# Kernel tuning notes

Hardware: AMD Instinct MI355X
Metric: run time of the kernel (lower is better)

The kernel has to match this reference:

```python
import jax, jax.numpy as jnp
import numpy as np

B, S, E, H = 8, 1024, 1024, 16
D = E // H            # head_dim = 64
L = 1024              # pos_max_len; rpe table rows = 2*L+1
SCALE = D ** 0.5


def setup_inputs() -> dict:
    key = jax.random.key(0)
    ks = jax.random.split(key, 7)
    x = jax.random.normal(ks[0], (B, S, E), dtype=jnp.float32)
    mask = jnp.tril(jnp.ones((S, S), dtype=bool))[None, None]  # causal [1,1,S,S]
    w = 1.0 / np.sqrt(E)
    Wq = jax.random.normal(ks[1], (E, E), dtype=jnp.float32) * w
    Wk = jax.random.normal(ks[2], (E, E), dtype=jnp.float32) * w
    Wv = jax.random.normal(ks[3], (E, E), dtype=jnp.float32) * w
    Wo = jax.random.normal(ks[4], (E, E), dtype=jnp.float32) * w
    pek_table = jax.random.normal(ks[5], (2 * L + 1, D), dtype=jnp.float32) / D ** 0.5
    pev_table = jax.random.normal(ks[6], (2 * L + 1, D), dtype=jnp.float32) / D ** 0.5
    return {"x": x, "mask": mask, "Wq": Wq, "Wk": Wk, "Wv": Wv, "Wo": Wo,
            "pek_table": pek_table, "pev_table": pev_table}


def reference(x, mask, Wq, Wk, Wv, Wo, pek_table, pev_table):
    # QKV projections (torch Linear: y = x @ W.T), reshaped to [B,H,S,D]
    q = (x @ Wq.T).reshape(B, S, H, D).transpose(0, 2, 1, 3)
    k = (x @ Wk.T).reshape(B, S, H, D).transpose(0, 2, 1, 3)
    v = (x @ Wv.T).reshape(B, S, H, D).transpose(0, 2, 1, 3)

    scores = jnp.einsum('bhsd,bhtd->bhst', q, k) / SCALE  # [B,H,S,S]

    # relative-position embeddings: rel[i,j] selects embedding for offset j-i
    pos = jnp.arange(S)
    rel = jnp.clip(pos[None, :] - pos[:, None] + L, 0, 2 * L)  # [S,S]
    pek = pek_table[rel]  # [S,S,D]
    pev = pev_table[rel]  # [S,S,D]

    # RPE score term, replicating torch view/transpose semantics exactly:
    # Q2: [B,S,H,D] -> [S,B,H,D] -> [S, B*H, D]
    q2 = (x @ Wq.T).reshape(B, S, H, D).transpose(1, 0, 2, 3).reshape(S, B * H, D)
    s2 = jnp.einsum('snd,std->snt', q2, pek)               # [S, B*H, S]
    s2 = s2.reshape(S, H, B, S).transpose(2, 1, 0, 3)      # torch .view(S,H,B,S).transpose(0,2)
    scores = scores + s2 / SCALE

    scores = jnp.where(mask, scores, -jnp.inf)
    attn = jax.nn.softmax(scores, axis=-1)                  # [B,H,S,S]

    out = jnp.einsum('bhst,bhtd->bhsd', attn, v)            # [B,H,S,D]

    # RPE value term: attn.transpose(0,2) -> [S,H,B,S] -> [S, H*B, S]
    a2 = attn.transpose(2, 1, 0, 3).reshape(S, H * B, S)
    o2 = jnp.einsum('snt,std->snd', a2, pev)                # [S, H*B, D]
    o2 = o2.reshape(S, H, B, D).transpose(2, 1, 0, 3)       # [B,H,S,D]
    out = out + o2

    out = out.transpose(0, 2, 1, 3).reshape(B, S, E) @ Wo.T
    return out
```

## Files before the change

kernel.cpp:

```cpp
#include <hip/hip_runtime.h>
#include <math.h>

#define NB 8
#define NS 1024
#define NE 1024
#define NH 16
#define ND 64
#define NL 1024

typedef __attribute__((ext_vector_type(8))) short short8;
typedef __attribute__((ext_vector_type(4))) float f32x4;
typedef __attribute__((ext_vector_type(16))) float f32x16;

__device__ __forceinline__ ushort f2bf(float f) {
    union { __bf16 h; ushort u; } v;
    v.h = (__bf16)f;
    return v.u;
}
__device__ __forceinline__ float bf2f(ushort u) {
    union { unsigned u; float f; } v; v.u = ((unsigned)u) << 16;
    return v.f;
}

__device__ __forceinline__ void stage16(const ushort* gsrc, ushort* lbase) {
    __builtin_amdgcn_global_load_lds((const __attribute__((address_space(1))) void*)gsrc,
                                     (__attribute__((address_space(3))) void*)lbase,
                                     16, 0, 0);
}

__global__ __launch_bounds__(256)
void cast_f2b4(const float* __restrict__ in, ushort* __restrict__ out, int n4) {
    int i = blockIdx.x * 256 + threadIdx.x;
    if (i >= n4) return;
    float4 v = ((const float4*)in)[i];
    ((ushort4*)out)[i] = make_ushort4(f2bf(v.x), f2bf(v.y), f2bf(v.z), f2bf(v.w));
}

__global__ __launch_bounds__(256)
void cast_w4(const float* __restrict__ Wq, const float* __restrict__ Wk,
             const float* __restrict__ Wv, const float* __restrict__ Wo,
             ushort* __restrict__ out) {
    int i = blockIdx.x * 256 + threadIdx.x;
    const int seg = i >> 18, j = i & 262143;
    const float* src = seg == 0 ? Wq : seg == 1 ? Wk : seg == 2 ? Wv : Wo;
    float4 v = ((const float4*)src)[j];
    ((ushort4*)out)[i] = make_ushort4(f2bf(v.x), f2bf(v.y), f2bf(v.z), f2bf(v.w));
}

__global__ __launch_bounds__(256)
void cast_pek(const float* __restrict__ pek, ushort* __restrict__ out, int n) {
    int i = blockIdx.x * 256 + threadIdx.x;
    if (i >= n) return;
    const int r = i >> 6, d = i & 63;
    out[(size_t)(d >> 4) * 32784 + (size_t)r * 16 + (d & 15)] = f2bf(pek[i]);
}

__global__ __launch_bounds__(256)
void cast_pevt(const float* __restrict__ pev, ushort* __restrict__ out) {
    int i = blockIdx.x * 256 + threadIdx.x;
    if (i >= 64 * 1056) return;
    const int d = i / 1056, r = i % 1056;
    const int m = r >> 5, cc = (r >> 4) & 1, hi = (r >> 3) & 1, j = r & 7;
    const int a = d >> 5, sl = d & 31;
    out[(size_t)m * 2048 + cc * 1024 + a * 512 + (sl * 2 + hi) * 8 + j] =
        f2bf(pev[(size_t)(r + 1) * ND + d]);
}

template<int MODE>
__global__ __launch_bounds__(256)
void gemm_mfma(const ushort* __restrict__ A, const ushort* __restrict__ W,
               float* __restrict__ Cf, ushort* __restrict__ Cb)
{
    constexpr int K = 1024;
    __shared__ __align__(16) ushort As[128 * 32];
    __shared__ __align__(16) ushort Bs[128 * 32];
    const int tid = threadIdx.x;
    const int w   = tid >> 6;
    const int l   = tid & 63;
    const int m0  = blockIdx.x * 128;
    const int n0  = blockIdx.y * 128;
    const int wr  = w >> 1, wc = w & 1;

    const int srow = 16 * w + (l >> 2);
    const int scol = (l & 3) * 8;
    const ushort* aptr = A + (size_t)(m0 + srow) * K + scol;
    const ushort* bptr = W + (size_t)(n0 + srow) * K + scol;
    ushort* asl = &As[w * 512];
    ushort* bsl = &Bs[w * 512];

    const int fl = l & 15, fk = (l >> 4) * 8;

    f32x4 acc[4][4] = {};

    for (int k0 = 0; k0 < K; k0 += 32) {
        __syncthreads();
        stage16(aptr + k0,                    asl);
        stage16(aptr + k0 + (size_t)64 * K,   asl + 2048);
        stage16(bptr + k0,                    bsl);
        stage16(bptr + k0 + (size_t)64 * K,   bsl + 2048);
        __syncthreads();

        short8 af[4], bf[4];
        #pragma unroll
        for (int i = 0; i < 4; ++i)
            af[i] = *(const short8*)&As[(wr * 64 + i * 16 + fl) * 32 + fk];
        #pragma unroll
        for (int j = 0; j < 4; ++j)
            bf[j] = *(const short8*)&Bs[(wc * 64 + j * 16 + fl) * 32 + fk];
        #pragma unroll
        for (int i = 0; i < 4; ++i)
            #pragma unroll
            for (int j = 0; j < 4; ++j)
                acc[i][j] = __builtin_amdgcn_mfma_f32_16x16x32_bf16(af[i], bf[j], acc[i][j], 0, 0, 0);
    }

    #pragma unroll
    for (int i = 0; i < 4; ++i) {
        #pragma unroll
        for (int j = 0; j < 4; ++j) {
            #pragma unroll
            for (int q = 0; q < 4; ++q) {
                const int m = m0 + wr * 64 + i * 16 + (l >> 4) * 4 + q;
                const int n = n0 + wc * 64 + j * 16 + fl;
                const float vv = acc[i][j][q];
                if (MODE == 0) {
                    const int b = m >> 10, s = m & 1023, h = n >> 6, d = n & 63;
                    Cb[(((size_t)b * NH + h) * NS + s) * ND + d] = f2bf(vv);
                } else if (MODE == 4) {
                    const int bh = (m >> 10) * 16 + (n >> 6), t = m & 1023, d = n & 63;
                    Cb[((size_t)bh * 4 + (d >> 4)) * 16384 + (size_t)t * 16 + (d & 15)] = f2bf(vv);
                } else if (MODE == 3) {
                    const int h = m >> 6, d = m & 63, b = n >> 10, s = n & 1023;
                    const int bh = b * 16 + h;
                    const int it = s >> 5, trel = s & 31;
                    const int c = trel >> 4, hi = (trel >> 3) & 1, jj = trel & 7;
                    const int a = d >> 5, sl = d & 31;
                    Cb[(size_t)bh * 65536 + it * 2048 +
                       ((a * 2 + c) * 64 + sl * 2 + hi) * 8 + jj] = f2bf(vv);
                } else {
                    Cf[(size_t)m * NE + n] = vv;
                }
            }
        }
    }
}

__global__ __launch_bounds__(64, 2)
void attn_mfma(const ushort* __restrict__ Qb, const ushort* __restrict__ Kf_,
               const ushort* __restrict__ Vf_, const ushort* __restrict__ PEKf,
               const ushort* __restrict__ PEVf, ushort* __restrict__ AO)
{
    const int idx = blockIdx.x;
    const int st  = 31 - (idx >> 7);
    const int bh  = idx & 127;
    const int b   = bh >> 4, h = bh & 15;
    const int n2  = h * NB + b;
    const int b2  = n2 >> 4, h2 = n2 & 15;
    const int s0  = st * 32;

    const int lane = threadIdx.x;
    const int sl   = lane & 31;
    const int hi   = lane >> 5;

    __shared__ __align__(16) ushort Mb[2][32][67];
    __shared__ __align__(16) ushort Pb[2][32][72];

    for (int t = lane; t < 2 * 32 * 72 / 2; t += 64) ((int*)Pb)[t] = 0;

    const ushort* qptr  = Qb + (((size_t)bh * NS) + s0 + sl) * ND + hi * 8;
    const ushort* q2ptr = Qb + ((((size_t)b2 * NH + h2) * NS) + s0 + sl) * ND + hi * 8;
    short8 qf[4], q2f[4];
    #pragma unroll
    for (int c = 0; c < 4; ++c) {
        qf[c]  = *(const short8*)(qptr  + 16 * c);
        q2f[c] = *(const short8*)(q2ptr + 16 * c);
    }

    const ushort* kfb  = Kf_ + (size_t)bh * 65536 + sl * 16 + hi * 8;
    const ushort* vfb  = Vf_ + (size_t)bh * 65536 + (sl * 2 + hi) * 8;
    const ushort* efb  = PEKf + sl * 16 + hi * 8;
    const ushort* pevw = PEVf + (size_t)(31 - st) * 2048 + (sl * 2 + hi) * 8;
    const int RBASE = NL - 31 - s0;

    auto mchunk = [&](int c, int dual, const short8* ef) {
        f32x16 cm = {};
        #pragma unroll
        for (int c4 = 0; c4 < 4; ++c4)
            cm = __builtin_amdgcn_mfma_f32_32x32x16_bf16(q2f[c4], ef[c4], cm, 0, 0, 0);
        #pragma unroll
        for (int q = 0; q < 16; ++q) {
            const int srow = (q & 3) + 8 * (q >> 2) + 4 * hi;
            const ushort bb = f2bf(cm[q]);
            Mb[c & 1][srow][sl] = bb;
            if (dual) Mb[(c + 1) & 1][srow][32 + sl] = bb;
        }
    };

    f32x16 acc0 = {}, acc1 = {};
    float mrow = -1e30f, lrow = 0.f;
    short8 kf[4], va[2][2], ea[4][2], efn[4];

    {
        short8 e0[4], e1[4];
        #pragma unroll
        for (int c4 = 0; c4 < 4; ++c4) {
            e0[c4] = *(const short8*)(efb + (size_t)c4 * 32784 + (size_t)RBASE * 16);
            e1[c4] = *(const short8*)(efb + (size_t)c4 * 32784 + (size_t)(RBASE + 32) * 16);
        }
        __builtin_amdgcn_s_setprio(1);
        mchunk(0, 0, e0);
        mchunk(1, 1, e1);
        __builtin_amdgcn_s_setprio(0);
    }
    #pragma unroll
    for (int c = 0; c < 4; ++c)
        kf[c] = *(const short8*)(kfb + c * 16384);
    #pragma unroll
    for (int c = 0; c < 2; ++c)
        #pragma unroll
        for (int a = 0; a < 2; ++a)
            va[c][a] = *(const short8*)(vfb + (a * 2 + c) * 512);
    if (st >= 1) {
        #pragma unroll
        for (int c4 = 0; c4 < 4; ++c4)
            efn[c4] = *(const short8*)(efb + (size_t)c4 * 32784 + (size_t)(RBASE + 64) * 16);
    }

    for (int i = 0; i <= st; ++i) {
        const int t0 = i * 32;
        const int p  = i & 1;

        f32x16 csw = {};
        __builtin_amdgcn_s_setprio(1);
        #pragma unroll
        for (int c = 0; c < 4; ++c)
            csw = __builtin_amdgcn_mfma_f32_32x32x16_bf16(kf[c], qf[c], csw, 0, 0, 0);
        __builtin_amdgcn_s_setprio(0);

        if (i < st) {
            #pragma unroll
            for (int c = 0; c < 4; ++c)
                kf[c] = *(const short8*)(kfb + c * 16384 + (size_t)(t0 + 32) * 16);
        }

        float sc[16];
        #pragma unroll
        for (int q = 0; q < 16; ++q) {
            const int trow = (q & 3) + 8 * (q >> 2) + 4 * hi;
            const int u = trow + 31 - sl;
            sc[q] = (csw[q] + bf2f(Mb[p][sl][u])) * 0.125f;
        }
        if (i == st) {
            #pragma unroll
            for (int q = 0; q < 16; ++q) {
                const int trow = (q & 3) + 8 * (q >> 2) + 4 * hi;
                if (t0 + trow > s0 + sl) sc[q] = -1e30f;
            }
        }
        float tm8[8], tm4[4];
        #pragma unroll
        for (int q = 0; q < 8; ++q) tm8[q] = fmaxf(sc[q], sc[q + 8]);
        #pragma unroll
        for (int q = 0; q < 4; ++q) tm4[q] = fmaxf(tm8[q], tm8[q + 4]);
        float tmax = fmaxf(fmaxf(tm4[0], tm4[1]), fmaxf(tm4[2], tm4[3]));

        if (i > 0) {
            __builtin_amdgcn_s_setprio(1);
            #pragma unroll
            for (int c = 0; c < 4; ++c) {
                short8 pskew = *(const short8*)&Pb[p ^ 1][sl][16 * c + 8 * hi];
                acc0 = __builtin_amdgcn_mfma_f32_32x32x16_bf16(ea[c][0], pskew, acc0, 0, 0, 0);
                acc1 = __builtin_amdgcn_mfma_f32_32x32x16_bf16(ea[c][1], pskew, acc1, 0, 0, 0);
            }
            __builtin_amdgcn_s_setprio(0);
        }

        #pragma unroll
        for (int c = 0; c < 4; ++c)
            #pragma unroll
            for (int a = 0; a < 2; ++a)
                ea[c][a] = *(const short8*)(pevw + (size_t)(i + (c >> 1)) * 2048 +
                                            (c & 1) * 1024 + a * 512);

        tmax = fmaxf(tmax, __shfl_xor(tmax, 32));
        if (!__all(tmax <= mrow + 8.f)) {
            const float mnew = fmaxf(mrow, tmax);
            const float r = __expf(mrow - mnew);
            lrow *= r;
            acc0 *= r; acc1 *= r;
            mrow = mnew;
        }
        float ps[16];
        #pragma unroll
        for (int q = 0; q < 16; ++q) ps[q] = __expf(sc[q] - mrow);
        float ls8[8], ls4[4];
        #pragma unroll
        for (int q = 0; q < 8; ++q) ls8[q] = ps[q] + ps[q + 8];
        #pragma unroll
        for (int q = 0; q < 4; ++q) ls4[q] = ls8[q] + ls8[q + 4];
        float lsum = (ls4[0] + ls4[1]) + (ls4[2] + ls4[3]);
        lsum += __shfl_xor(lsum, 32);
        lrow += lsum;

        #pragma unroll
        for (int q = 0; q < 16; ++q) {
            const int trow = (q & 3) + 8 * (q >> 2) + 4 * hi;
            Pb[p][sl][trow + 31 - sl] = f2bf(ps[q]);
        }

        if (i < st) {
            __builtin_amdgcn_s_setprio(1);
            mchunk(i + 2, 1, efn);
            __builtin_amdgcn_s_setprio(0);
            if (i + 1 < st) {
                #pragma unroll
                for (int c4 = 0; c4 < 4; ++c4)
                    efn[c4] = *(const short8*)(efb + (size_t)c4 * 32784 +
                                               (size_t)(RBASE + 32 * (i + 3)) * 16);
            }
        }

        float sh[16];
        #pragma unroll
        for (int q = 0; q < 16; ++q) sh[q] = __shfl_xor(ps[q], 32);
        __builtin_amdgcn_s_setprio(1);
        #pragma unroll
        for (int c = 0; c < 2; ++c) {
            short8 bfrag;
            #pragma unroll
            for (int j = 0; j < 8; ++j) {
                float pv;
                if (j < 4) pv = hi ? sh[8 * c + 4 + j] : ps[8 * c + j];
                else       pv = hi ? ps[8 * c + j]     : sh[8 * c + j - 4];
                bfrag[j] = (short)f2bf(pv);
            }
            acc0 = __builtin_amdgcn_mfma_f32_32x32x16_bf16(va[c][0], bfrag, acc0, 0, 0, 0);
            acc1 = __builtin_amdgcn_mfma_f32_32x32x16_bf16(va[c][1], bfrag, acc1, 0, 0, 0);
        }
        __builtin_amdgcn_s_setprio(0);

        if (i < st) {
            #pragma unroll
            for (int c = 0; c < 2; ++c)
                #pragma unroll
                for (int a = 0; a < 2; ++a)
                    va[c][a] = *(const short8*)(vfb + (size_t)(i + 1) * 2048 + (a * 2 + c) * 512);
        }
    }

    {
        __builtin_amdgcn_s_setprio(1);
        #pragma unroll
        for (int c = 0; c < 4; ++c) {
            short8 pskew = *(const short8*)&Pb[st & 1][sl][16 * c + 8 * hi];
            acc0 = __builtin_amdgcn_mfma_f32_32x32x16_bf16(ea[c][0], pskew, acc0, 0, 0, 0);
            acc1 = __builtin_amdgcn_mfma_f32_32x32x16_bf16(ea[c][1], pskew, acc1, 0, 0, 0);
        }
        __builtin_amdgcn_s_setprio(0);
    }

    const float inv = 1.0f / lrow;
    ushort* orow = AO + ((size_t)b * NS + s0 + sl) * NE + h * ND;
    #pragma unroll
    for (int g = 0; g < 4; ++g) {
        ushort4 o0 = make_ushort4(f2bf(acc0[4*g+0]*inv), f2bf(acc0[4*g+1]*inv),
                                  f2bf(acc0[4*g+2]*inv), f2bf(acc0[4*g+3]*inv));
        ushort4 o1 = make_ushort4(f2bf(acc1[4*g+0]*inv), f2bf(acc1[4*g+1]*inv),
                                  f2bf(acc1[4*g+2]*inv), f2bf(acc1[4*g+3]*inv));
        *(ushort4*)&orow[8 * g + 4 * hi]      = o0;
        *(ushort4*)&orow[8 * g + 4 * hi + 32] = o1;
    }
}

extern "C" void kernel_launch(void* const* d_in, const int* in_sizes, int n_in,
                              void* d_out, int out_size, void* d_ws, size_t ws_size,
                              hipStream_t stream) {
    const float* x   = (const float*)d_in[0];
    const float* Wq  = (const float*)d_in[2];
    const float* Wk  = (const float*)d_in[3];
    const float* Wv  = (const float*)d_in[4];
    const float* Wo  = (const float*)d_in[5];
    const float* pek = (const float*)d_in[6];
    const float* pev = (const float*)d_in[7];

    ushort* ws16 = (ushort*)d_ws;
    size_t off = 0;
    ushort* xb    = ws16 + off; off += (size_t)8388608;
    ushort* Wqb   = ws16 + off; off += (size_t)1048576;
    ushort* Wkb   = ws16 + off; off += (size_t)1048576;
    ushort* Wvb   = ws16 + off; off += (size_t)1048576;
    ushort* Wob   = ws16 + off; off += (size_t)1048576;
    ushort* Qb    = ws16 + off; off += (size_t)8388608;
    ushort* Kfm   = ws16 + off; off += (size_t)8388608;
    ushort* Vfm   = ws16 + off; off += (size_t)8388608;
    ushort* PEKf  = ws16 + off; off += (size_t)131136;
    ushort* PEVf  = ws16 + off; off += (size_t)67584;
    ushort* aob   = ws16 + off; off += (size_t)8388608;
    float*  out   = (float*)d_out;

    dim3 blk(256);
    cast_f2b4<<<8192, blk, 0, stream>>>(x, xb, 2097152);
    cast_w4<<<4096, blk, 0, stream>>>(Wq, Wk, Wv, Wo, Wqb);
    cast_pek<<<(2049 * 64 + 255) / 256, blk, 0, stream>>>(pek, PEKf, 2049 * 64);
    cast_pevt<<<(64 * 1056 + 255) / 256, blk, 0, stream>>>(pev, PEVf);

    gemm_mfma<0><<<dim3(64, 8), blk, 0, stream>>>(xb, Wqb, nullptr, Qb);
    gemm_mfma<4><<<dim3(64, 8), blk, 0, stream>>>(xb, Wkb, nullptr, Kfm);
    gemm_mfma<3><<<dim3(8, 64), blk, 0, stream>>>(Wvb, xb, nullptr, Vfm);

    attn_mfma<<<dim3(4096), dim3(64), 0, stream>>>(Qb, Kfm, Vfm, PEKf, PEVf, aob);

    gemm_mfma<1><<<dim3(64, 8), blk, 0, stream>>>(aob, Wob, out, nullptr);
}
```

Measured before the change: 234.1 us.

## Cut register pressure in RPE attention loop to allow three waves per SIMD

Raises launch bounds from two to three waves per SIMD. To make that fit, the PEV-term MFMA is computed in the same iteration instead of one step late, so P only needs a single LDS buffer. The PEK fragments are now loaded inside mchunk rather than prefetched, and the PEV fragments are kept as a rolling prev/new pair instead of eight registers. This should free VGPRs and LDS for higher occupancy, at the cost of less load latency hiding because the prefetches are dropped. It also adds an LDS read-after-write dependency within the iteration.

```diff
diff --git a/kernel.cpp b/kernel.cpp
--- a/kernel.cpp
+++ b/kernel.cpp
@@ -145,7 +145,7 @@
     }
 }
 
-__global__ __launch_bounds__(64, 2)
+__global__ __launch_bounds__(64, 3)
 void attn_mfma(const ushort* __restrict__ Qb, const ushort* __restrict__ Kf_,
                const ushort* __restrict__ Vf_, const ushort* __restrict__ PEKf,
                const ushort* __restrict__ PEVf, ushort* __restrict__ AO)
@@ -163,9 +163,9 @@
     const int hi   = lane >> 5;
 
     __shared__ __align__(16) ushort Mb[2][32][67];
-    __shared__ __align__(16) ushort Pb[2][32][72];
-
-    for (int t = lane; t < 2 * 32 * 72 / 2; t += 64) ((int*)Pb)[t] = 0;
+    __shared__ __align__(16) ushort Pb[32][72];
+
+    for (int t = lane; t < 32 * 72 / 2; t += 64) ((int*)Pb)[t] = 0;
 
     const ushort* qptr  = Qb + (((size_t)bh * NS) + s0 + sl) * ND + hi * 8;
     const ushort* q2ptr = Qb + ((((size_t)b2 * NH + h2) * NS) + s0 + sl) * ND + hi * 8;
@@ -182,11 +182,14 @@
     const ushort* pevw = PEVf + (size_t)(31 - st) * 2048 + (sl * 2 + hi) * 8;
     const int RBASE = NL - 31 - s0;
 
-    auto mchunk = [&](int c, int dual, const short8* ef) {
+    auto mchunk = [&](int c, int dual) {
         f32x16 cm = {};
         #pragma unroll
-        for (int c4 = 0; c4 < 4; ++c4)
-            cm = __builtin_amdgcn_mfma_f32_32x32x16_bf16(q2f[c4], ef[c4], cm, 0, 0, 0);
+        for (int c4 = 0; c4 < 4; ++c4) {
+            short8 ef = *(const short8*)(efb + (size_t)c4 * 32784 +
+                                         (size_t)(RBASE + 32 * c) * 16);
+            cm = __builtin_amdgcn_mfma_f32_32x32x16_bf16(q2f[c4], ef, cm, 0, 0, 0);
+        }
         #pragma unroll
         for (int q = 0; q < 16; ++q) {
             const int srow = (q & 3) + 8 * (q >> 2) + 4 * hi;
@@ -198,37 +201,33 @@
 
     f32x16 acc0 = {}, acc1 = {};
     float mrow = -1e30f, lrow = 0.f;
-    short8 kf[4], va[2][2], ea[4][2], efn[4];
-
-    {
-        short8 e0[4], e1[4];
-        #pragma unroll
-        for (int c4 = 0; c4 < 4; ++c4) {
-            e0[c4] = *(const short8*)(efb + (size_t)c4 * 32784 + (size_t)RBASE * 16);
-            e1[c4] = *(const short8*)(efb + (size_t)c4 * 32784 + (size_t)(RBASE + 32) * 16);
-        }
-        __builtin_amdgcn_s_setprio(1);
-        mchunk(0, 0, e0);
-        mchunk(1, 1, e1);
-        __builtin_amdgcn_s_setprio(0);
-    }
+    short8 kf[4], va[2][2], eaPrev[2][2], eaNew[2][2];
+
+    __builtin_amdgcn_s_setprio(1);
+    mchunk(0, 0);
+    mchunk(1, 1);
+    __builtin_amdgcn_s_setprio(0);
     #pragma unroll
     for (int c = 0; c < 4; ++c)
         kf[c] = *(const short8*)(kfb + c * 16384);
     #pragma unroll
     for (int c = 0; c < 2; ++c)
         #pragma unroll
-        for (int a = 0; a < 2; ++a)
-            va[c][a] = *(const short8*)(vfb + (a * 2 + c) * 512);
-    if (st >= 1) {
-        #pragma unroll
-        for (int c4 = 0; c4 < 4; ++c4)
-            efn[c4] = *(const short8*)(efb + (size_t)c4 * 32784 + (size_t)(RBASE + 64) * 16);
-    }
+        for (int a = 0; a < 2; ++a) {
+            va[c][a]     = *(const short8*)(vfb + (a * 2 + c) * 512);
+            eaPrev[c][a] = *(const short8*)(pevw + c * 1024 + a * 512);
+        }
 
     for (int i = 0; i <= st; ++i) {
         const int t0 = i * 32;
         const int p  = i & 1;
+
+        #pragma unroll
+        for (int c = 0; c < 2; ++c)
+            #pragma unroll
+            for (int a = 0; a < 2; ++a)
+                eaNew[c][a] = *(const short8*)(pevw + (size_t)(i + 1) * 2048 +
+                                               c * 1024 + a * 512);
 
         f32x16 csw = {};
         __builtin_amdgcn_s_setprio(1);
@@ -263,24 +262,6 @@
         #pragma unroll
         for (int q = 0; q < 4; ++q) tm4[q] = fmaxf(tm8[q], tm8[q + 4]);
         float tmax = fmaxf(fmaxf(tm4[0], tm4[1]), fmaxf(tm4[2], tm4[3]));
-
-        if (i > 0) {
-            __builtin_amdgcn_s_setprio(1);
-            #pragma unroll
-            for (int c = 0; c < 4; ++c) {
-                short8 pskew = *(const short8*)&Pb[p ^ 1][sl][16 * c + 8 * hi];
-                acc0 = __builtin_amdgcn_mfma_f32_32x32x16_bf16(ea[c][0], pskew, acc0, 0, 0, 0);
-                acc1 = __builtin_amdgcn_mfma_f32_32x32x16_bf16(ea[c][1], pskew, acc1, 0, 0, 0);
-            }
-            __builtin_amdgcn_s_setprio(0);
-        }
-
-        #pragma unroll
-        for (int c = 0; c < 4; ++c)
-            #pragma unroll
-            for (int a = 0; a < 2; ++a)
-                ea[c][a] = *(const short8*)(pevw + (size_t)(i + (c >> 1)) * 2048 +
-                                            (c & 1) * 1024 + a * 512);
 
         tmax = fmaxf(tmax, __shfl_xor(tmax, 32));
         if (!__all(tmax <= mrow + 8.f)) {
@@ -305,40 +286,54 @@
         #pragma unroll
         for (int q = 0; q < 16; ++q) {
             const int trow = (q & 3) + 8 * (q >> 2) + 4 * hi;
-            Pb[p][sl][trow + 31 - sl] = f2bf(ps[q]);
+            Pb[sl][trow + 31 - sl] = f2bf(ps[q]);
         }
 
         if (i < st) {
             __builtin_amdgcn_s_setprio(1);
-            mchunk(i + 2, 1, efn);
+            mchunk(i + 2, 1);
             __builtin_amdgcn_s_setprio(0);
-            if (i + 1 < st) {
-                #pragma unroll
-                for (int c4 = 0; c4 < 4; ++c4)
-                    efn[c4] = *(const short8*)(efb + (size_t)c4 * 32784 +
-                                               (size_t)(RBASE + 32 * (i + 3)) * 16);
-            }
-        }
-
-        float sh[16];
-        #pragma unroll
-        for (int q = 0; q < 16; ++q) sh[q] = __shfl_xor(ps[q], 32);
+        }
+
         __builtin_amdgcn_s_setprio(1);
         #pragma unroll
         for (int c = 0; c < 2; ++c) {
+            float shc[8];
+            #pragma unroll
+            for (int j = 0; j < 8; ++j) shc[j] = __shfl_xor(ps[8 * c + j], 32);
             short8 bfrag;
             #pragma unroll
             for (int j = 0; j < 8; ++j) {
                 float pv;
-                if (j < 4) pv = hi ? sh[8 * c + 4 + j] : ps[8 * c + j];
-                else       pv = hi ? ps[8 * c + j]     : sh[8 * c + j - 4];
+                if (j < 4) pv = hi ? shc[4 + j]     : ps[8 * c + j];
+                else       pv = hi ? ps[8 * c + j]  : shc[j - 4];
                 bfrag[j] = (short)f2bf(pv);
             }
             acc0 = __builtin_amdgcn_mfma_f32_32x32x16_bf16(va[c][0], bfrag, acc0, 0, 0, 0);
             acc1 = __builtin_amdgcn_mfma_f32_32x32x16_bf16(va[c][1], bfrag, acc1, 0, 0, 0);
         }
+
+        {
+            short8 pk0 = *(const short8*)&Pb[sl][0 + 8 * hi];
+            acc0 = __builtin_amdgcn_mfma_f32_32x32x16_bf16(eaPrev[0][0], pk0, acc0, 0, 0, 0);
+            acc1 = __builtin_amdgcn_mfma_f32_32x32x16_bf16(eaPrev[0][1], pk0, acc1, 0, 0, 0);
+            short8 pk1 = *(const short8*)&Pb[sl][16 + 8 * hi];
+            acc0 = __builtin_amdgcn_mfma_f32_32x32x16_bf16(eaPrev[1][0], pk1, acc0, 0, 0, 0);
+            acc1 = __builtin_amdgcn_mfma_f32_32x32x16_bf16(eaPrev[1][1], pk1, acc1, 0, 0, 0);
+            short8 pk2 = *(const short8*)&Pb[sl][32 + 8 * hi];
+            acc0 = __builtin_amdgcn_mfma_f32_32x32x16_bf16(eaNew[0][0], pk2, acc0, 0, 0, 0);
+            acc1 = __builtin_amdgcn_mfma_f32_32x32x16_bf16(eaNew[0][1], pk2, acc1, 0, 0, 0);
+            short8 pk3 = *(const short8*)&Pb[sl][48 + 8 * hi];
+            acc0 = __builtin_amdgcn_mfma_f32_32x32x16_bf16(eaNew[1][0], pk3, acc0, 0, 0, 0);
+            acc1 = __builtin_amdgcn_mfma_f32_32x32x16_bf16(eaNew[1][1], pk3, acc1, 0, 0, 0);
+        }
         __builtin_amdgcn_s_setprio(0);
 
+        #pragma unroll
+        for (int c = 0; c < 2; ++c)
+            #pragma unroll
+            for (int a = 0; a < 2; ++a)
+                eaPrev[c][a] = eaNew[c][a];
         if (i < st) {
             #pragma unroll
             for (int c = 0; c < 2; ++c)
@@ -346,17 +341,6 @@
                 for (int a = 0; a < 2; ++a)
                     va[c][a] = *(const short8*)(vfb + (size_t)(i + 1) * 2048 + (a * 2 + c) * 512);
         }
-    }
-
-    {
-        __builtin_amdgcn_s_setprio(1);
-        #pragma unroll
-        for (int c = 0; c < 4; ++c) {
-            short8 pskew = *(const short8*)&Pb[st & 1][sl][16 * c + 8 * hi];
-            acc0 = __builtin_amdgcn_mfma_f32_32x32x16_bf16(ea[c][0], pskew, acc0, 0, 0, 0);
-            acc1 = __builtin_amdgcn_mfma_f32_32x32x16_bf16(ea[c][1], pskew, acc1, 0, 0, 0);
-        }
-        __builtin_amdgcn_s_setprio(0);
     }
 
     const float inv = 1.0f / lrow;
```

Result: slower. 243.7 us (+4.1%).
